# Performance work log

Hardware: AMD Instinct MI355X
Metric: run time of the kernel (lower is better)

The kernel has to match this reference:

```python
import jax, jax.numpy as jnp
import numpy as np

N_NODES = 100000
N_EDGES = 3200000
N_GRAPHS = 256
IN_CH = 8
HID = 64


def _gcn_conv(x, W, b, src, dst, n):
    # PyG GCNConv default: add self-loops, symmetric normalization.
    # out_i = sum_{j->i} d_i^-1/2 d_j^-1/2 (xW)_j + (1/d_i)(xW)_i + b
    xw = x @ W                                     # [N, out]
    deg = jax.ops.segment_sum(jnp.ones_like(dst, dtype=xw.dtype), dst,
                              num_segments=n) + 1.0  # +1 for self-loop
    dinv = jax.lax.rsqrt(deg)
    norm = dinv[src] * dinv[dst]                   # [E]
    agg = jax.ops.segment_sum(xw[src] * norm[:, None], dst, num_segments=n)
    agg = agg + xw * (1.0 / deg)[:, None]          # self-loop term (norm = 1/deg)
    return agg + b


def setup_inputs() -> dict:
    key = jax.random.key(0)
    ks = jax.random.split(key, 12)
    x = jax.random.normal(ks[0], (N_NODES, IN_CH), dtype=jnp.float32)
    edge_index = jax.random.randint(ks[1], (2, N_EDGES), 0, N_NODES, dtype=jnp.int64)
    batch = jnp.sort(jax.random.randint(ks[2], (N_NODES,), 0, N_GRAPHS, dtype=jnp.int64))

    def glorot(k, fan_in, fan_out):
        s = jnp.sqrt(2.0 / (fan_in + fan_out)).astype(jnp.float32)
        return jax.random.normal(k, (fan_in, fan_out), dtype=jnp.float32) * s

    return {
        "x": x, "edge_index": edge_index, "batch": batch,
        "W1": glorot(ks[3], IN_CH, HID), "b1": jnp.zeros((HID,), jnp.float32),
        "W2": glorot(ks[4], HID, 2 * HID), "b2": jnp.zeros((2 * HID,), jnp.float32),
        "W3": glorot(ks[5], 2 * HID, HID), "b3": jnp.zeros((HID,), jnp.float32),
        "Wl1": glorot(ks[6], HID, HID // 2), "bl1": jnp.zeros((HID // 2,), jnp.float32),
        "Wl2": glorot(ks[7], HID // 2, 1), "bl2": jnp.zeros((1,), jnp.float32),
    }


def reference(x, edge_index, batch, W1, b1, W2, b2, W3, b3, Wl1, bl1, Wl2, bl2):
    src, dst = edge_index[0], edge_index[1]
    h = jax.nn.relu(_gcn_conv(x, W1, b1, src, dst, N_NODES))
    h = jax.nn.relu(_gcn_conv(h, W2, b2, src, dst, N_NODES))
    h = jax.nn.relu(_gcn_conv(h, W3, b3, src, dst, N_NODES))
    # global mean pool over graphs
    sums = jax.ops.segment_sum(h, batch, num_segments=N_GRAPHS)
    cnts = jax.ops.segment_sum(jnp.ones((N_NODES,), h.dtype), batch, num_segments=N_GRAPHS)
    g = sums / jnp.maximum(cnts, 1.0)[:, None]     # [G, HID]
    g = jax.nn.relu(g @ Wl1 + bl1)
    out = g @ Wl2 + bl2                            # [G, 1]
    return out[:, 0]
```

## Files before the change

### kernel.cpp

```cpp
#include <hip/hip_runtime.h>
#include <hip/hip_bf16.h>

#define N_NODES 100000
#define N_EDGES 3200000
#define N_GRAPHS 256
#define NB_BUCKETS 196
#define BSHIFT 9
#define NBLK 256
#define SCAN_BLKS 49
#define CSR_CAP 22528

#define OFF_SUMS      0u
#define OFF_CNTF      65536u
#define ZERO_BYTES    66560u
#define OFF_HIST      66560u
#define OFF_BSUM      267264u
#define OFF_ROWPTR    267776u
#define OFF_DINV      668160u
#define OFF_COL       1068544u
#define OFF_XS1       13868544u
#define OFF_BUFQ      20268544u
#define OFF_BUFR      45868544u
#define OFF_BUFP      71468544u
#define OFF_PAIRS     OFF_BUFP

__device__ __forceinline__ unsigned short f2bf(float f) {
    unsigned u = __float_as_uint(f);
    return (unsigned short)((u + 0x7fffu + ((u >> 16) & 1u)) >> 16);
}

__device__ __forceinline__ void acc_bf8(uint4 v, float m, float* a) {
    a[0] += m * __uint_as_float(v.x << 16);
    a[1] += m * __uint_as_float(v.x & 0xffff0000u);
    a[2] += m * __uint_as_float(v.y << 16);
    a[3] += m * __uint_as_float(v.y & 0xffff0000u);
    a[4] += m * __uint_as_float(v.z << 16);
    a[5] += m * __uint_as_float(v.z & 0xffff0000u);
    a[6] += m * __uint_as_float(v.w << 16);
    a[7] += m * __uint_as_float(v.w & 0xffff0000u);
}

__global__ __launch_bounds__(256) void hist_kernel(const int* __restrict__ dst,
                                                   int* __restrict__ hist,
                                                   int* __restrict__ zbase,
                                                   int E, int epb) {
    __shared__ int h[NB_BUCKETS];
    int t = threadIdx.x, blk = blockIdx.x;
    int gid = blk * 256 + t;
    if (gid < (int)(ZERO_BYTES / 4)) zbase[gid] = 0;
    if (t < NB_BUCKETS) h[t] = 0;
    __syncthreads();
    int e0 = blk * epb, e1 = min(e0 + epb, E);
    for (int e = e0 + t; e < e1; e += 256)
        atomicAdd(&h[__builtin_nontemporal_load(&dst[e]) >> BSHIFT], 1);
    __syncthreads();
    if (t < NB_BUCKETS) hist[t * NBLK + blk] = h[t];
}

__global__ __launch_bounds__(1024) void scanhA_kernel(int* __restrict__ hist,
                                                      int* __restrict__ bsum) {
    __shared__ int s[1024];
    int t = threadIdx.x;
    int i = blockIdx.x * 1024 + t;
    int v = hist[i];
    s[t] = v;
    __syncthreads();
    for (int off = 1; off < 1024; off <<= 1) {
        int add = (t >= off) ? s[t - off] : 0;
        __syncthreads();
        s[t] += add;
        __syncthreads();
    }
    hist[i] = s[t] - v;
    if (t == 1023) bsum[blockIdx.x] = s[t];
}

__global__ __launch_bounds__(256) void bin_kernel(const int* __restrict__ src,
                                                  const int* __restrict__ dst,
                                                  const int* __restrict__ hist,
                                                  const int* __restrict__ bsum,
                                                  int* __restrict__ packed, int E, int epb) {
    __shared__ int cur[NB_BUCKETS];
    __shared__ int boffL[SCAN_BLKS];
    int t = threadIdx.x, blk = blockIdx.x;
    if (t < 64) {
        int orig = (t < SCAN_BLKS) ? bsum[t] : 0;
        int v = orig;
        for (int off = 1; off < 64; off <<= 1) {
            int up = __shfl_up(v, off);
            if (t >= off) v += up;
        }
        if (t < SCAN_BLKS) boffL[t] = v - orig;
    }
    __syncthreads();
    if (t < NB_BUCKETS) {
        int i = t * NBLK + blk;
        cur[t] = hist[i] + boffL[i >> 10];
    }
    __syncthreads();
    int e0 = blk * epb, e1 = min(e0 + epb, E);
    for (int e = e0 + t; e < e1; e += 256) {
        int d = __builtin_nontemporal_load(&dst[e]);
        int sv = __builtin_nontemporal_load(&src[e]);
        int pos = atomicAdd(&cur[d >> BSHIFT], 1);
        packed[pos] = ((d & 511) << 17) | sv;
    }
}

__global__ __launch_bounds__(512) void csr_kernel(const int* __restrict__ packed,
                                                  const int* __restrict__ hist,
                                                  const int* __restrict__ bsum,
                                                  const float* __restrict__ x,
                                                  int* __restrict__ row_ptr,
                                                  float* __restrict__ dinv,
                                                  unsigned short* __restrict__ xs1,
                                                  int* __restrict__ col, int E) {
    __shared__ int cntL[512];
    __shared__ int rsL[512];
    __shared__ int fillL[512];
    __shared__ int boffL[SCAN_BLKS];
    __shared__ int srcL[CSR_CAP];
    int t = threadIdx.x, b = blockIdx.x;
    int lo = b << BSHIFT;
    int nloc = min(512, N_NODES - lo);
    cntL[t] = 0;
    fillL[t] = 0;
    if (t < 64) {
        int orig = (t < SCAN_BLKS) ? bsum[t] : 0;
        int v = orig;
        for (int off = 1; off < 64; off <<= 1) {
            int up = __shfl_up(v, off);
            if (t >= off) v += up;
        }
        if (t < SCAN_BLKS) boffL[t] = v - orig;
    }
    __syncthreads();
    int i0 = b * NBLK;
    int start = hist[i0] + boffL[i0 >> 10];
    int end;
    if (b == NB_BUCKETS - 1) end = E;
    else {
        int i1 = (b + 1) * NBLK;
        end = hist[i1] + boffL[i1 >> 10];
    }
    for (int e = start + t; e < end; e += 512)
        atomicAdd(&cntL[packed[e] >> 17], 1);
    __syncthreads();
    int v = cntL[t];
    __syncthreads();
    for (int off = 1; off < 512; off <<= 1) {
        int add = (t >= off) ? cntL[t - off] : 0;
        __syncthreads();
        cntL[t] += add;
        __syncthreads();
    }
    int rowstart = start + cntL[t] - v;
    rsL[t] = rowstart;
    if (t < nloc) {
        int node = lo + t;
        row_ptr[node] = rowstart;
        float d = rsqrtf((float)(v + 1));
        dinv[node] = d;
        const float4* xv = reinterpret_cast<const float4*>(x) + node * 2;
        float4 xa = xv[0], xb = xv[1];
        uint4 p;
        p.x = (unsigned)f2bf(xa.x * d) | ((unsigned)f2bf(xa.y * d) << 16);
        p.y = (unsigned)f2bf(xa.z * d) | ((unsigned)f2bf(xa.w * d) << 16);
        p.z = (unsigned)f2bf(xb.x * d) | ((unsigned)f2bf(xb.y * d) << 16);
        p.w = (unsigned)f2bf(xb.z * d) | ((unsigned)f2bf(xb.w * d) << 16);
        *reinterpret_cast<uint4*>(&xs1[node * 8]) = p;
    }
    if (b == NB_BUCKETS - 1 && t == 0) row_ptr[N_NODES] = E;
    __syncthreads();
    for (int e = start + t; e < end; e += 512) {
        int p = packed[e];
        int dl = p >> 17;
        int pos = rsL[dl] + atomicAdd(&fillL[dl], 1);
        int rel = pos - start;
        if (rel < CSR_CAP) srcL[rel] = p & 0x1FFFF;
        else col[pos] = p & 0x1FFFF;
    }
    __syncthreads();
    int lim = min(end - start, CSR_CAP);
    for (int i = t; i < lim; i += 512)
        col[start + i] = srcL[i];
}

__global__ __launch_bounds__(256) void agg8g1_kernel(
        const unsigned short* __restrict__ xs, const int* __restrict__ row_ptr,
        const int* __restrict__ col, const float* __restrict__ dinv,
        const float* __restrict__ W1, const float* __restrict__ b1,
        unsigned short* __restrict__ xs2, int n) {
    int wave = threadIdx.x >> 6;
    int node = blockIdx.x * 4 + wave;
    if (node >= n) return;
    int lane = threadIdx.x & 63;
    float w[8];
    float bias = b1[lane];
#pragma unroll
    for (int k = 0; k < 8; ++k) w[k] = W1[k * 64 + lane];
    int e0 = row_ptr[node], e1 = row_ptr[node + 1];
    float a[8] = {0.f, 0.f, 0.f, 0.f, 0.f, 0.f, 0.f, 0.f};
    uint4 sv = *reinterpret_cast<const uint4*>(&xs[node * 8]);
    int base = e0;
    for (; base + 64 <= e1; base += 64) {
        int c = __builtin_nontemporal_load(&col[base + lane]);
        uint4 v = *reinterpret_cast<const uint4*>(&xs[c * 8]);
        acc_bf8(v, 1.f, a);
    }
    if (base < e1) {
        int e = base + lane;
        int c = __builtin_nontemporal_load(&col[min(e, e1 - 1)]);
        uint4 v = *reinterpret_cast<const uint4*>(&xs[c * 8]);
        acc_bf8(v, (e < e1) ? 1.f : 0.f, a);
    }
    acc_bf8(sv, (lane == 0) ? 1.f : 0.f, a);
#pragma unroll
    for (int k = 0; k < 8; ++k) {
        a[k] += __shfl_xor(a[k], 1);
        a[k] += __shfl_xor(a[k], 2);
        a[k] += __shfl_xor(a[k], 4);
    }
    float v8 = a[lane & 7];
    v8 += __shfl_xor(v8, 8);
    v8 += __shfl_xor(v8, 16);
    v8 += __shfl_xor(v8, 32);
    float d = dinv[node];
    float acc = bias;
#pragma unroll
    for (int k = 0; k < 8; ++k) acc += (__shfl(v8, k) * d) * w[k];
    xs2[node * 64 + lane] = f2bf(d * fmaxf(acc, 0.0f));
}

template <bool BF16OUT>
__global__ __launch_bounds__(256) void agg64bf_kernel(
        const unsigned short* __restrict__ xs, const int* __restrict__ row_ptr,
        const int* __restrict__ col, const float* __restrict__ dinv,
        float* __restrict__ z, int n) {
    int wave = threadIdx.x >> 6;
    int node = blockIdx.x * 4 + wave;
    if (node >= n) return;
    int lane = threadIdx.x & 63;
    int j = lane >> 3, l = lane & 7;
    int e0 = row_ptr[node], e1 = row_ptr[node + 1];
    float a[8] = {0.f, 0.f, 0.f, 0.f, 0.f, 0.f, 0.f, 0.f};
    uint4 sv = *reinterpret_cast<const uint4*>(&xs[node * 64 + 8 * l]);
    int base = e0;
    for (; e1 - base > 48; base += 32) {
        int s0 = __builtin_nontemporal_load(&col[base + j]);
        int s1 = __builtin_nontemporal_load(&col[base + 8 + j]);
        int s2 = __builtin_nontemporal_load(&col[base + 16 + j]);
        int s3 = __builtin_nontemporal_load(&col[base + 24 + j]);
        uint4 v0 = *reinterpret_cast<const uint4*>(&xs[s0 * 64 + 8 * l]);
        uint4 v1 = *reinterpret_cast<const uint4*>(&xs[s1 * 64 + 8 * l]);
        uint4 v2 = *reinterpret_cast<const uint4*>(&xs[s2 * 64 + 8 * l]);
        uint4 v3 = *reinterpret_cast<const uint4*>(&xs[s3 * 64 + 8 * l]);
        acc_bf8(v0, 1.f, a); acc_bf8(v1, 1.f, a);
        acc_bf8(v2, 1.f, a); acc_bf8(v3, 1.f, a);
    }
    int rem = e1 - base;
    if (rem > 0) {
        int e1m1 = e1 - 1;
        bool g4 = rem > 32, g5 = rem > 40;
        int i0 = base + j,      i1 = base + 8 + j;
        int i2 = base + 16 + j, i3 = base + 24 + j;
        int i4 = base + 32 + j, i5 = base + 40 + j;
        int c0 = __builtin_nontemporal_load(&col[min(i0, e1m1)]);
        int c1 = __builtin_nontemporal_load(&col[min(i1, e1m1)]);
        int c2 = __builtin_nontemporal_load(&col[min(i2, e1m1)]);
        int c3 = __builtin_nontemporal_load(&col[min(i3, e1m1)]);
        int c4 = 0, c5 = 0;
        if (g4) c4 = __builtin_nontemporal_load(&col[min(i4, e1m1)]);
        if (g5) c5 = __builtin_nontemporal_load(&col[min(i5, e1m1)]);
        uint4 v0 = *reinterpret_cast<const uint4*>(&xs[c0 * 64 + 8 * l]);
        uint4 v1 = *reinterpret_cast<const uint4*>(&xs[c1 * 64 + 8 * l]);
        uint4 v2 = *reinterpret_cast<const uint4*>(&xs[c2 * 64 + 8 * l]);
        uint4 v3 = *reinterpret_cast<const uint4*>(&xs[c3 * 64 + 8 * l]);
        uint4 v4, v5;
        if (g4) v4 = *reinterpret_cast<const uint4*>(&xs[c4 * 64 + 8 * l]);
        if (g5) v5 = *reinterpret_cast<const uint4*>(&xs[c5 * 64 + 8 * l]);
        acc_bf8(v0, (i0 < e1) ? 1.f : 0.f, a);
        acc_bf8(v1, (i1 < e1) ? 1.f : 0.f, a);
        acc_bf8(v2, (i2 < e1) ? 1.f : 0.f, a);
        acc_bf8(v3, (i3 < e1) ? 1.f : 0.f, a);
        if (g4) acc_bf8(v4, (i4 < e1) ? 1.f : 0.f, a);
        if (g5) acc_bf8(v5, (i5 < e1) ? 1.f : 0.f, a);
    }
    acc_bf8(sv, (j == 0) ? 1.f : 0.f, a);
#pragma unroll
    for (int k = 0; k < 8; ++k) {
        a[k] += __shfl_xor(a[k], 8);
        a[k] += __shfl_xor(a[k], 16);
        a[k] += __shfl_xor(a[k], 32);
    }
    if (j == 0) {
        float d = dinv[node];
        if constexpr (BF16OUT) {
            unsigned short* zh = reinterpret_cast<unsigned short*>(z);
            uint4 p;
            p.x = (unsigned)f2bf(a[0] * d) | ((unsigned)f2bf(a[1] * d) << 16);
            p.y = (unsigned)f2bf(a[2] * d) | ((unsigned)f2bf(a[3] * d) << 16);
            p.z = (unsigned)f2bf(a[4] * d) | ((unsigned)f2bf(a[5] * d) << 16);
            p.w = (unsigned)f2bf(a[6] * d) | ((unsigned)f2bf(a[7] * d) << 16);
            *reinterpret_cast<uint4*>(&zh[node * 64 + 8 * l]) = p;
        } else {
            float4 r0 = {a[0] * d, a[1] * d, a[2] * d, a[3] * d};
            float4 r1 = {a[4] * d, a[5] * d, a[6] * d, a[7] * d};
            *reinterpret_cast<float4*>(&z[node * 64 + 8 * l]) = r0;
            *reinterpret_cast<float4*>(&z[node * 64 + 8 * l + 4]) = r1;
        }
    }
}

template <int K, int M, bool BIAS, bool RELU, bool SCALE, bool BF16IN, bool BF16OUT>
__global__ __launch_bounds__(256) void gemm_kernel(
        const float* __restrict__ X, const float* __restrict__ W,
        const float* __restrict__ b, const float* __restrict__ dinv,
        float* __restrict__ Y, int nrows) {
    constexpr int CG = M / 4;
    constexpr int RG = 256 / CG;
    constexpr int ROWS = RG * 4;
    constexpr int XSTR = K + 4;
    __shared__ float Wl[K * M];
    __shared__ float Xl[ROWS * XSTR];
    __shared__ float Bl[M];
    int tid = threadIdx.x;
    {
        const float4* Wv = reinterpret_cast<const float4*>(W);
        float4* Wlv = reinterpret_cast<float4*>(Wl);
        for (int i = tid; i < K * M / 4; i += 256) Wlv[i] = Wv[i];
    }
    if (tid < M) Bl[tid] = BIAS ? b[tid] : 0.0f;
    int cg = tid % CG;
    int rg = tid / CG;
    int ntiles = (nrows + ROWS - 1) / ROWS;
    for (int tile = blockIdx.x; tile < ntiles; tile += gridDim.x) {
        int row0 = tile * ROWS;
        __syncthreads();
        {
            int base4 = row0 * (K / 4);
            int tot4 = nrows * (K / 4);
            for (int i = tid; i < ROWS * K / 4; i += 256) {
                float4 v = {0.f, 0.f, 0.f, 0.f};
                if (base4 + i < tot4) {
                    if constexpr (BF16IN) {
                        uint2 raw = reinterpret_cast<const uint2*>(X)[base4 + i];
                        v.x = __uint_as_float(raw.x << 16);
                        v.y = __uint_as_float(raw.x & 0xffff0000u);
                        v.z = __uint_as_float(raw.y << 16);
                        v.w = __uint_as_float(raw.y & 0xffff0000u);
                    } else {
                        v = reinterpret_cast<const float4*>(X)[base4 + i];
                    }
                }
                int rr = i / (K / 4), kk = i % (K / 4);
                *reinterpret_cast<float4*>(&Xl[rr * XSTR + kk * 4]) = v;
            }
        }
        __syncthreads();
        float4 acc[4];
#pragma unroll
        for (int rr = 0; rr < 4; ++rr)
            acc[rr] = *reinterpret_cast<const float4*>(&Bl[cg * 4]);
#pragma unroll 1
        for (int k = 0; k < K; k += 4) {
            const float4 w0 = *reinterpret_cast<const float4*>(&Wl[(k + 0) * M + cg * 4]);
            const float4 w1 = *reinterpret_cast<const float4*>(&Wl[(k + 1) * M + cg * 4]);
            const float4 w2 = *reinterpret_cast<const float4*>(&Wl[(k + 2) * M + cg * 4]);
            const float4 w3 = *reinterpret_cast<const float4*>(&Wl[(k + 3) * M + cg * 4]);
#pragma unroll
            for (int rr = 0; rr < 4; ++rr) {
                const float4 xv = *reinterpret_cast<const float4*>(
                    &Xl[(rg * 4 + rr) * XSTR + k]);
                acc[rr].x += xv.x * w0.x + xv.y * w1.x + xv.z * w2.x + xv.w * w3.x;
                acc[rr].y += xv.x * w0.y + xv.y * w1.y + xv.z * w2.y + xv.w * w3.y;
                acc[rr].z += xv.x * w0.z + xv.y * w1.z + xv.z * w2.z + xv.w * w3.z;
                acc[rr].w += xv.x * w0.w + xv.y * w1.w + xv.z * w2.w + xv.w * w3.w;
            }
        }
#pragma unroll
        for (int rr = 0; rr < 4; ++rr) {
            int row = row0 + rg * 4 + rr;
            if (row < nrows) {
                float4 a = acc[rr];
                if constexpr (RELU) {
                    a.x = fmaxf(a.x, 0.f); a.y = fmaxf(a.y, 0.f);
                    a.z = fmaxf(a.z, 0.f); a.w = fmaxf(a.w, 0.f);
                }
                if constexpr (SCALE) {
                    float d = dinv[row];
                    a.x *= d; a.y *= d; a.z *= d; a.w *= d;
                }
                if constexpr (BF16OUT) {
                    unsigned short* Yh = reinterpret_cast<unsigned short*>(Y);
                    uint2 p;
                    p.x = (unsigned)f2bf(a.x) | ((unsigned)f2bf(a.y) << 16);
                    p.y = (unsigned)f2bf(a.z) | ((unsigned)f2bf(a.w) << 16);
                    *reinterpret_cast<uint2*>(&Yh[row * M + cg * 4]) = p;
                } else {
                    *reinterpret_cast<float4*>(&Y[row * M + cg * 4]) = a;
                }
            }
        }
    }
}

#define POOL_NPB 128
__global__ __launch_bounds__(256) void pool_kernel(
        const float* __restrict__ z3, const float* __restrict__ b3,
        const int* __restrict__ batch, float* __restrict__ sums,
        float* __restrict__ cntf, int n) {
    int wave = threadIdx.x >> 6;
    int lane = threadIdx.x & 63;
    int node0 = blockIdx.x * POOL_NPB + wave * 32;
    int nodeEnd = min(node0 + 32, n);
    if (node0 >= n) return;
    float bias = b3[lane];
    float acc = 0.0f, cnt = 0.0f;
    int curg = -1;
    for (int node = node0; node < nodeEnd; ++node) {
        int g = batch[node];
        if (g != curg) {
            if (curg >= 0) {
                atomicAdd(&sums[curg * 64 + lane], acc);
                if (lane == 0) atomicAdd(&cntf[curg], cnt);
            }
            curg = g; acc = 0.0f; cnt = 0.0f;
        }
        acc += fmaxf(__builtin_nontemporal_load(&z3[node * 64 + lane]) + bias, 0.0f);
        cnt += 1.0f;
    }
    if (curg >= 0) {
        atomicAdd(&sums[curg * 64 + lane], acc);
        if (lane == 0) atomicAdd(&cntf[curg], cnt);
    }
}

__global__ void mlp_kernel(const float* __restrict__ sums, const float* __restrict__ cntf,
                           const float* __restrict__ Wl1, const float* __restrict__ bl1,
                           const float* __restrict__ Wl2, const float* __restrict__ bl2,
                           float* __restrict__ out) {
    __shared__ float gv[64];
    __shared__ float hid[32];
    int g = blockIdx.x, t = threadIdx.x;
    float denom = fmaxf(cntf[g], 1.0f);
    gv[t] = sums[g * 64 + t] / denom;
    __syncthreads();
    if (t < 32) {
        float a = bl1[t];
#pragma unroll
        for (int k = 0; k < 64; ++k) a += gv[k] * Wl1[k * 32 + t];
        hid[t] = fmaxf(a, 0.0f);
    }
    __syncthreads();
    if (t == 0) {
        float o = bl2[0];
#pragma unroll
        for (int k = 0; k < 32; ++k) o += hid[k] * Wl2[k];
        out[g] = o;
    }
}

extern "C" void kernel_launch(void* const* d_in, const int* in_sizes, int n_in,
                              void* d_out, int out_size, void* d_ws, size_t ws_size,
                              hipStream_t stream) {
    const float* x   = (const float*)d_in[0];
    const int* ei    = (const int*)d_in[1];
    const int* batch = (const int*)d_in[2];
    const float* W1  = (const float*)d_in[3];
    const float* b1  = (const float*)d_in[4];
    const float* W2  = (const float*)d_in[5];
    const float* b2  = (const float*)d_in[6];
    const float* W3  = (const float*)d_in[7];
    const float* b3  = (const float*)d_in[8];
    const float* Wl1 = (const float*)d_in[9];
    const float* bl1 = (const float*)d_in[10];
    const float* Wl2 = (const float*)d_in[11];
    const float* bl2 = (const float*)d_in[12];
    float* out = (float*)d_out;

    const int N = N_NODES;
    const int E = in_sizes[1] / 2;
    const int* src = ei;
    const int* dst = ei + E;

    char* ws = (char*)d_ws;
    float* sums    = (float*)(ws + OFF_SUMS);
    float* cntf    = (float*)(ws + OFF_CNTF);
    int*   hist    = (int*)(ws + OFF_HIST);
    int*   bsum    = (int*)(ws + OFF_BSUM);
    int*   row_ptr = (int*)(ws + OFF_ROWPTR);
    float* dinv    = (float*)(ws + OFF_DINV);
    int*   col     = (int*)(ws + OFF_COL);
    unsigned short* xs1 = (unsigned short*)(ws + OFF_XS1);
    float* bufQ    = (float*)(ws + OFF_BUFQ);
    float* bufR    = (float*)(ws + OFF_BUFR);
    float* bufP    = (float*)(ws + OFF_BUFP);
    int*   packed  = (int*)(ws + OFF_PAIRS);

    int epb = (E + NBLK - 1) / NBLK;
    hist_kernel<<<NBLK, 256, 0, stream>>>(dst, hist, (int*)ws, E, epb);
    scanhA_kernel<<<SCAN_BLKS, 1024, 0, stream>>>(hist, bsum);
    bin_kernel<<<NBLK, 256, 0, stream>>>(src, dst, hist, bsum, packed, E, epb);
    csr_kernel<<<NB_BUCKETS, 512, 0, stream>>>(packed, hist, bsum, x,
                                               row_ptr, dinv, xs1, col, E);

    agg8g1_kernel<<<(N + 3) / 4, 256, 0, stream>>>(xs1, row_ptr, col, dinv, W1, b1,
                                                   (unsigned short*)bufQ, N);

    agg64bf_kernel<true><<<(N + 3) / 4, 256, 0, stream>>>(
        (const unsigned short*)bufQ, row_ptr, col, dinv, bufR, N);
    gemm_kernel<64, 128, true, true, false, true, true><<<3125, 256, 0, stream>>>(
        bufR, W2, b2, nullptr, bufP, N);

    gemm_kernel<128, 64, false, false, true, true, true><<<1563, 256, 0, stream>>>(
        bufP, W3, nullptr, dinv, bufR, N);
    agg64bf_kernel<false><<<(N + 3) / 4, 256, 0, stream>>>(
        (const unsigned short*)bufR, row_ptr, col, dinv, bufQ, N);

    pool_kernel<<<(N + POOL_NPB - 1) / POOL_NPB, 256, 0, stream>>>(bufQ, b3, batch, sums, cntf, N);
    mlp_kernel<<<N_GRAPHS, 64, 0, stream>>>(sums, cntf, Wl1, bl1, Wl2, bl2, out);
}
```

Baseline: 405.9 us.

## Replace two-level bucketed CSR build with global-atomic degree count and scatter

Replaces the bucket histogram, bin and per-bucket LDS CSR construction with a direct scheme. Per-node degrees are counted with global atomics, a two-level prefix scan produces row pointers, and a scatter kernel places each edge's source through a per-node atomic cursor. This removes the intermediate packed buffer and the LDS sort pass, but it adds millions of scattered global atomics and random column writes. It also adds more kernel launches and makes the order of columns within each row nondeterministic.

```diff
diff --git a/kernel.cpp b/kernel.cpp
--- a/kernel.cpp
+++ b/kernel.cpp
@@ -4,25 +4,21 @@
 #define N_NODES 100000
 #define N_EDGES 3200000
 #define N_GRAPHS 256
-#define NB_BUCKETS 196
-#define BSHIFT 9
-#define NBLK 256
-#define SCAN_BLKS 49
-#define CSR_CAP 22528
+#define SCAN1_BLKS 98
 
 #define OFF_SUMS      0u
 #define OFF_CNTF      65536u
-#define ZERO_BYTES    66560u
-#define OFF_HIST      66560u
-#define OFF_BSUM      267264u
-#define OFF_ROWPTR    267776u
-#define OFF_DINV      668160u
-#define OFF_COL       1068544u
-#define OFF_XS1       13868544u
+#define OFF_DEG       66560u
+#define ZERO_BYTES    466576u
+#define OFF_BSUM2     466576u
+#define OFF_ROWPTR    467088u
+#define OFF_CURS      867104u
+#define OFF_DINV      1267104u
+#define OFF_COL       1667104u
+#define OFF_XS1       14467104u
 #define OFF_BUFQ      20268544u
 #define OFF_BUFR      45868544u
 #define OFF_BUFP      71468544u
-#define OFF_PAIRS     OFF_BUFP
 
 __device__ __forceinline__ unsigned short f2bf(float f) {
     unsigned u = __float_as_uint(f);
@@ -40,29 +36,25 @@
     a[7] += m * __uint_as_float(v.w & 0xffff0000u);
 }
 
-__global__ __launch_bounds__(256) void hist_kernel(const int* __restrict__ dst,
-                                                   int* __restrict__ hist,
-                                                   int* __restrict__ zbase,
-                                                   int E, int epb) {
-    __shared__ int h[NB_BUCKETS];
-    int t = threadIdx.x, blk = blockIdx.x;
-    int gid = blk * 256 + t;
+__global__ __launch_bounds__(256) void zero_kernel(int* __restrict__ zbase) {
+    int gid = blockIdx.x * 256 + threadIdx.x;
     if (gid < (int)(ZERO_BYTES / 4)) zbase[gid] = 0;
-    if (t < NB_BUCKETS) h[t] = 0;
-    __syncthreads();
-    int e0 = blk * epb, e1 = min(e0 + epb, E);
-    for (int e = e0 + t; e < e1; e += 256)
-        atomicAdd(&h[__builtin_nontemporal_load(&dst[e]) >> BSHIFT], 1);
-    __syncthreads();
-    if (t < NB_BUCKETS) hist[t * NBLK + blk] = h[t];
-}
-
-__global__ __launch_bounds__(1024) void scanhA_kernel(int* __restrict__ hist,
-                                                      int* __restrict__ bsum) {
+}
+
+__global__ __launch_bounds__(256) void deg_kernel(const int* __restrict__ dst,
+                                                  int* __restrict__ deg, int E) {
+    int stride = gridDim.x * 256;
+    for (int e = blockIdx.x * 256 + threadIdx.x; e < E; e += stride)
+        atomicAdd(&deg[__builtin_nontemporal_load(&dst[e])], 1);
+}
+
+__global__ __launch_bounds__(1024) void scan1_kernel(const int* __restrict__ deg,
+                                                     int* __restrict__ rp,
+                                                     int* __restrict__ bsum, int n) {
     __shared__ int s[1024];
     int t = threadIdx.x;
     int i = blockIdx.x * 1024 + t;
-    int v = hist[i];
+    int v = (i < n) ? deg[i] : 0;
     s[t] = v;
     __syncthreads();
     for (int off = 1; off < 1024; off <<= 1) {
@@ -71,119 +63,64 @@
         s[t] += add;
         __syncthreads();
     }
-    hist[i] = s[t] - v;
+    if (i < n) rp[i] = s[t] - v;
     if (t == 1023) bsum[blockIdx.x] = s[t];
 }
 
-__global__ __launch_bounds__(256) void bin_kernel(const int* __restrict__ src,
-                                                  const int* __restrict__ dst,
-                                                  const int* __restrict__ hist,
-                                                  const int* __restrict__ bsum,
-                                                  int* __restrict__ packed, int E, int epb) {
-    __shared__ int cur[NB_BUCKETS];
-    __shared__ int boffL[SCAN_BLKS];
+__global__ __launch_bounds__(128) void scan2_kernel(int* __restrict__ bsum) {
+    __shared__ int s[128];
+    int t = threadIdx.x;
+    int v = (t < SCAN1_BLKS) ? bsum[t] : 0;
+    s[t] = v;
+    __syncthreads();
+    for (int off = 1; off < 128; off <<= 1) {
+        int add = (t >= off) ? s[t - off] : 0;
+        __syncthreads();
+        s[t] += add;
+        __syncthreads();
+    }
+    if (t < SCAN1_BLKS) bsum[t] = s[t] - v;
+}
+
+__global__ __launch_bounds__(1024) void fin_kernel(const int* __restrict__ bsum,
+                                                   const int* __restrict__ deg,
+                                                   const float* __restrict__ x,
+                                                   int* __restrict__ rp,
+                                                   int* __restrict__ cursor,
+                                                   float* __restrict__ dinv,
+                                                   unsigned short* __restrict__ xs1,
+                                                   int n, int E) {
     int t = threadIdx.x, blk = blockIdx.x;
-    if (t < 64) {
-        int orig = (t < SCAN_BLKS) ? bsum[t] : 0;
-        int v = orig;
-        for (int off = 1; off < 64; off <<= 1) {
-            int up = __shfl_up(v, off);
-            if (t >= off) v += up;
-        }
-        if (t < SCAN_BLKS) boffL[t] = v - orig;
-    }
-    __syncthreads();
-    if (t < NB_BUCKETS) {
-        int i = t * NBLK + blk;
-        cur[t] = hist[i] + boffL[i >> 10];
-    }
-    __syncthreads();
-    int e0 = blk * epb, e1 = min(e0 + epb, E);
-    for (int e = e0 + t; e < e1; e += 256) {
-        int d = __builtin_nontemporal_load(&dst[e]);
-        int sv = __builtin_nontemporal_load(&src[e]);
-        int pos = atomicAdd(&cur[d >> BSHIFT], 1);
-        packed[pos] = ((d & 511) << 17) | sv;
-    }
-}
-
-__global__ __launch_bounds__(512) void csr_kernel(const int* __restrict__ packed,
-                                                  const int* __restrict__ hist,
-                                                  const int* __restrict__ bsum,
-                                                  const float* __restrict__ x,
-                                                  int* __restrict__ row_ptr,
-                                                  float* __restrict__ dinv,
-                                                  unsigned short* __restrict__ xs1,
-                                                  int* __restrict__ col, int E) {
-    __shared__ int cntL[512];
-    __shared__ int rsL[512];
-    __shared__ int fillL[512];
-    __shared__ int boffL[SCAN_BLKS];
-    __shared__ int srcL[CSR_CAP];
-    int t = threadIdx.x, b = blockIdx.x;
-    int lo = b << BSHIFT;
-    int nloc = min(512, N_NODES - lo);
-    cntL[t] = 0;
-    fillL[t] = 0;
-    if (t < 64) {
-        int orig = (t < SCAN_BLKS) ? bsum[t] : 0;
-        int v = orig;
-        for (int off = 1; off < 64; off <<= 1) {
-            int up = __shfl_up(v, off);
-            if (t >= off) v += up;
-        }
-        if (t < SCAN_BLKS) boffL[t] = v - orig;
-    }
-    __syncthreads();
-    int i0 = b * NBLK;
-    int start = hist[i0] + boffL[i0 >> 10];
-    int end;
-    if (b == NB_BUCKETS - 1) end = E;
-    else {
-        int i1 = (b + 1) * NBLK;
-        end = hist[i1] + boffL[i1 >> 10];
-    }
-    for (int e = start + t; e < end; e += 512)
-        atomicAdd(&cntL[packed[e] >> 17], 1);
-    __syncthreads();
-    int v = cntL[t];
-    __syncthreads();
-    for (int off = 1; off < 512; off <<= 1) {
-        int add = (t >= off) ? cntL[t - off] : 0;
-        __syncthreads();
-        cntL[t] += add;
-        __syncthreads();
-    }
-    int rowstart = start + cntL[t] - v;
-    rsL[t] = rowstart;
-    if (t < nloc) {
-        int node = lo + t;
-        row_ptr[node] = rowstart;
-        float d = rsqrtf((float)(v + 1));
-        dinv[node] = d;
-        const float4* xv = reinterpret_cast<const float4*>(x) + node * 2;
+    int i = blk * 1024 + t;
+    if (i < n) {
+        int rpv = rp[i] + bsum[blk];
+        rp[i] = rpv;
+        cursor[i] = rpv;
+        float d = rsqrtf((float)(deg[i] + 1));
+        dinv[i] = d;
+        const float4* xv = reinterpret_cast<const float4*>(x) + i * 2;
         float4 xa = xv[0], xb = xv[1];
         uint4 p;
         p.x = (unsigned)f2bf(xa.x * d) | ((unsigned)f2bf(xa.y * d) << 16);
         p.y = (unsigned)f2bf(xa.z * d) | ((unsigned)f2bf(xa.w * d) << 16);
         p.z = (unsigned)f2bf(xb.x * d) | ((unsigned)f2bf(xb.y * d) << 16);
         p.w = (unsigned)f2bf(xb.z * d) | ((unsigned)f2bf(xb.w * d) << 16);
-        *reinterpret_cast<uint4*>(&xs1[node * 8]) = p;
-    }
-    if (b == NB_BUCKETS - 1 && t == 0) row_ptr[N_NODES] = E;
-    __syncthreads();
-    for (int e = start + t; e < end; e += 512) {
-        int p = packed[e];
-        int dl = p >> 17;
-        int pos = rsL[dl] + atomicAdd(&fillL[dl], 1);
-        int rel = pos - start;
-        if (rel < CSR_CAP) srcL[rel] = p & 0x1FFFF;
-        else col[pos] = p & 0x1FFFF;
-    }
-    __syncthreads();
-    int lim = min(end - start, CSR_CAP);
-    for (int i = t; i < lim; i += 512)
-        col[start + i] = srcL[i];
+        *reinterpret_cast<uint4*>(&xs1[i * 8]) = p;
+    }
+    if (i == 0) rp[n] = E;
+}
+
+__global__ __launch_bounds__(256) void scatter_kernel(const int* __restrict__ src,
+                                                      const int* __restrict__ dst,
+                                                      int* __restrict__ cursor,
+                                                      int* __restrict__ col, int E) {
+    int stride = gridDim.x * 256;
+    for (int e = blockIdx.x * 256 + threadIdx.x; e < E; e += stride) {
+        int d = __builtin_nontemporal_load(&dst[e]);
+        int s = __builtin_nontemporal_load(&src[e]);
+        int pos = atomicAdd(&cursor[d], 1);
+        __builtin_nontemporal_store(s, &col[pos]);
+    }
 }
 
 __global__ __launch_bounds__(256) void agg8g1_kernel(
@@ -487,23 +424,24 @@
     char* ws = (char*)d_ws;
     float* sums    = (float*)(ws + OFF_SUMS);
     float* cntf    = (float*)(ws + OFF_CNTF);
-    int*   hist    = (int*)(ws + OFF_HIST);
-    int*   bsum    = (int*)(ws + OFF_BSUM);
+    int*   deg     = (int*)(ws + OFF_DEG);
+    int*   bsum2   = (int*)(ws + OFF_BSUM2);
     int*   row_ptr = (int*)(ws + OFF_ROWPTR);
+    int*   cursor  = (int*)(ws + OFF_CURS);
     float* dinv    = (float*)(ws + OFF_DINV);
     int*   col     = (int*)(ws + OFF_COL);
     unsigned short* xs1 = (unsigned short*)(ws + OFF_XS1);
     float* bufQ    = (float*)(ws + OFF_BUFQ);
     float* bufR    = (float*)(ws + OFF_BUFR);
     float* bufP    = (float*)(ws + OFF_BUFP);
-    int*   packed  = (int*)(ws + OFF_PAIRS);
-
-    int epb = (E + NBLK - 1) / NBLK;
-    hist_kernel<<<NBLK, 256, 0, stream>>>(dst, hist, (int*)ws, E, epb);
-    scanhA_kernel<<<SCAN_BLKS, 1024, 0, stream>>>(hist, bsum);
-    bin_kernel<<<NBLK, 256, 0, stream>>>(src, dst, hist, bsum, packed, E, epb);
-    csr_kernel<<<NB_BUCKETS, 512, 0, stream>>>(packed, hist, bsum, x,
-                                               row_ptr, dinv, xs1, col, E);
+
+    zero_kernel<<<456, 256, 0, stream>>>((int*)ws);
+    deg_kernel<<<1024, 256, 0, stream>>>(dst, deg, E);
+    scan1_kernel<<<SCAN1_BLKS, 1024, 0, stream>>>(deg, row_ptr, bsum2, N);
+    scan2_kernel<<<1, 128, 0, stream>>>(bsum2);
+    fin_kernel<<<SCAN1_BLKS, 1024, 0, stream>>>(bsum2, deg, x, row_ptr, cursor,
+                                                dinv, xs1, N, E);
+    scatter_kernel<<<1024, 256, 0, stream>>>(src, dst, cursor, col, E);
 
     agg8g1_kernel<<<(N + 3) / 4, 256, 0, stream>>>(xs1, row_ptr, col, dinv, W1, b1,
                                                    (unsigned short*)bufQ, N);
```

Measured after the change: 728.3 us. 79.4% more time.

## Replace FP32 SIMT GEMMs with bf16 MFMA matrix-core GEMMs

Applied to the files above, without the earlier changes.

Replaces the shared-memory FP32 FMA GEMM for the layer-2 and layer-3 dense transforms with a kernel using the bf16 16x16x32 MFMA instruction. Each wave loads A fragments directly from global memory, and the weights are converted to bf16 and transposed into LDS per block. The goal is to cut the ALU cost of the two dense GEMMs. Weights are now also rounded to bf16, which adds precision loss. The aggregation kernel gains an unused node-range parameter.

```diff
diff --git a/kernel.cpp b/kernel.cpp
--- a/kernel.cpp
+++ b/kernel.cpp
@@ -23,6 +23,9 @@
 #define OFF_BUFR      45868544u
 #define OFF_BUFP      71468544u
 #define OFF_PAIRS     OFF_BUFP
+
+typedef __attribute__((ext_vector_type(8))) short bf16x8;
+typedef __attribute__((ext_vector_type(4))) float f32x4;
 
 __device__ __forceinline__ unsigned short f2bf(float f) {
     unsigned u = __float_as_uint(f);
@@ -236,10 +239,10 @@
 __global__ __launch_bounds__(256) void agg64bf_kernel(
         const unsigned short* __restrict__ xs, const int* __restrict__ row_ptr,
         const int* __restrict__ col, const float* __restrict__ dinv,
-        float* __restrict__ z, int n) {
+        float* __restrict__ z, int n0, int n1) {
     int wave = threadIdx.x >> 6;
-    int node = blockIdx.x * 4 + wave;
-    if (node >= n) return;
+    int node = n0 + blockIdx.x * 4 + wave;
+    if (node >= n1) return;
     int lane = threadIdx.x & 63;
     int j = lane >> 3, l = lane & 7;
     int e0 = row_ptr[node], e1 = row_ptr[node + 1];
@@ -312,94 +315,59 @@
     }
 }
 
-template <int K, int M, bool BIAS, bool RELU, bool SCALE, bool BF16IN, bool BF16OUT>
-__global__ __launch_bounds__(256) void gemm_kernel(
-        const float* __restrict__ X, const float* __restrict__ W,
+template <int K, int M, bool BIAS, bool RELU, bool SCALE, bool BF16OUT>
+__global__ __launch_bounds__(256) void mgemm_kernel(
+        const unsigned short* __restrict__ X, const float* __restrict__ W,
         const float* __restrict__ b, const float* __restrict__ dinv,
         float* __restrict__ Y, int nrows) {
-    constexpr int CG = M / 4;
-    constexpr int RG = 256 / CG;
-    constexpr int ROWS = RG * 4;
-    constexpr int XSTR = K + 4;
-    __shared__ float Wl[K * M];
-    __shared__ float Xl[ROWS * XSTR];
-    __shared__ float Bl[M];
+    constexpr int KP = K + 8;
+    constexpr int NT = M / 16;
+    constexpr int KS = K / 32;
+    __shared__ unsigned short Wt[M * KP];
     int tid = threadIdx.x;
-    {
-        const float4* Wv = reinterpret_cast<const float4*>(W);
-        float4* Wlv = reinterpret_cast<float4*>(Wl);
-        for (int i = tid; i < K * M / 4; i += 256) Wlv[i] = Wv[i];
-    }
-    if (tid < M) Bl[tid] = BIAS ? b[tid] : 0.0f;
-    int cg = tid % CG;
-    int rg = tid / CG;
-    int ntiles = (nrows + ROWS - 1) / ROWS;
-    for (int tile = blockIdx.x; tile < ntiles; tile += gridDim.x) {
-        int row0 = tile * ROWS;
-        __syncthreads();
-        {
-            int base4 = row0 * (K / 4);
-            int tot4 = nrows * (K / 4);
-            for (int i = tid; i < ROWS * K / 4; i += 256) {
-                float4 v = {0.f, 0.f, 0.f, 0.f};
-                if (base4 + i < tot4) {
-                    if constexpr (BF16IN) {
-                        uint2 raw = reinterpret_cast<const uint2*>(X)[base4 + i];
-                        v.x = __uint_as_float(raw.x << 16);
-                        v.y = __uint_as_float(raw.x & 0xffff0000u);
-                        v.z = __uint_as_float(raw.y << 16);
-                        v.w = __uint_as_float(raw.y & 0xffff0000u);
-                    } else {
-                        v = reinterpret_cast<const float4*>(X)[base4 + i];
-                    }
-                }
-                int rr = i / (K / 4), kk = i % (K / 4);
-                *reinterpret_cast<float4*>(&Xl[rr * XSTR + kk * 4]) = v;
-            }
-        }
-        __syncthreads();
-        float4 acc[4];
-#pragma unroll
-        for (int rr = 0; rr < 4; ++rr)
-            acc[rr] = *reinterpret_cast<const float4*>(&Bl[cg * 4]);
-#pragma unroll 1
-        for (int k = 0; k < K; k += 4) {
-            const float4 w0 = *reinterpret_cast<const float4*>(&Wl[(k + 0) * M + cg * 4]);
-            const float4 w1 = *reinterpret_cast<const float4*>(&Wl[(k + 1) * M + cg * 4]);
-            const float4 w2 = *reinterpret_cast<const float4*>(&Wl[(k + 2) * M + cg * 4]);
-            const float4 w3 = *reinterpret_cast<const float4*>(&Wl[(k + 3) * M + cg * 4]);
-#pragma unroll
-            for (int rr = 0; rr < 4; ++rr) {
-                const float4 xv = *reinterpret_cast<const float4*>(
-                    &Xl[(rg * 4 + rr) * XSTR + k]);
-                acc[rr].x += xv.x * w0.x + xv.y * w1.x + xv.z * w2.x + xv.w * w3.x;
-                acc[rr].y += xv.x * w0.y + xv.y * w1.y + xv.z * w2.y + xv.w * w3.y;
-                acc[rr].z += xv.x * w0.z + xv.y * w1.z + xv.z * w2.z + xv.w * w3.z;
-                acc[rr].w += xv.x * w0.w + xv.y * w1.w + xv.z * w2.w + xv.w * w3.w;
-            }
-        }
-#pragma unroll
-        for (int rr = 0; rr < 4; ++rr) {
-            int row = row0 + rg * 4 + rr;
-            if (row < nrows) {
-                float4 a = acc[rr];
-                if constexpr (RELU) {
-                    a.x = fmaxf(a.x, 0.f); a.y = fmaxf(a.y, 0.f);
-                    a.z = fmaxf(a.z, 0.f); a.w = fmaxf(a.w, 0.f);
-                }
-                if constexpr (SCALE) {
-                    float d = dinv[row];
-                    a.x *= d; a.y *= d; a.z *= d; a.w *= d;
-                }
-                if constexpr (BF16OUT) {
-                    unsigned short* Yh = reinterpret_cast<unsigned short*>(Y);
-                    uint2 p;
-                    p.x = (unsigned)f2bf(a.x) | ((unsigned)f2bf(a.y) << 16);
-                    p.y = (unsigned)f2bf(a.z) | ((unsigned)f2bf(a.w) << 16);
-                    *reinterpret_cast<uint2*>(&Yh[row * M + cg * 4]) = p;
-                } else {
-                    *reinterpret_cast<float4*>(&Y[row * M + cg * 4]) = a;
-                }
+    for (int i = tid; i < K * M; i += 256) {
+        int k = i / M, m = i % M;
+        Wt[m * KP + k] = f2bf(W[i]);
+    }
+    __syncthreads();
+    int wave = tid >> 6, lane = tid & 63;
+    int row0 = blockIdx.x * 64 + wave * 16;
+    int hl = lane >> 4, ll = lane & 15;
+    int arow = min(row0 + ll, nrows - 1);
+    bf16x8 afrag[KS];
+#pragma unroll
+    for (int ks = 0; ks < KS; ++ks)
+        afrag[ks] = *reinterpret_cast<const bf16x8*>(&X[arow * K + ks * 32 + hl * 8]);
+    f32x4 acc[NT];
+#pragma unroll
+    for (int nt = 0; nt < NT; ++nt) {
+        float bv = BIAS ? b[nt * 16 + ll] : 0.0f;
+        acc[nt] = {bv, bv, bv, bv};
+    }
+#pragma unroll
+    for (int nt = 0; nt < NT; ++nt) {
+#pragma unroll
+        for (int ks = 0; ks < KS; ++ks) {
+            bf16x8 bfrag = *reinterpret_cast<const bf16x8*>(
+                &Wt[(nt * 16 + ll) * KP + ks * 32 + hl * 8]);
+            acc[nt] = __builtin_amdgcn_mfma_f32_16x16x32_bf16(
+                afrag[ks], bfrag, acc[nt], 0, 0, 0);
+        }
+    }
+#pragma unroll
+    for (int r = 0; r < 4; ++r) {
+        int row = row0 + hl * 4 + r;
+        if (row < nrows) {
+            float d = SCALE ? dinv[row] : 1.0f;
+#pragma unroll
+            for (int nt = 0; nt < NT; ++nt) {
+                float v = acc[nt][r];
+                if constexpr (RELU) v = fmaxf(v, 0.0f);
+                if constexpr (SCALE) v *= d;
+                if constexpr (BF16OUT)
+                    reinterpret_cast<unsigned short*>(Y)[row * M + nt * 16 + ll] = f2bf(v);
+                else
+                    Y[row * M + nt * 16 + ll] = v;
             }
         }
     }
@@ -509,14 +477,14 @@
                                                    (unsigned short*)bufQ, N);
 
     agg64bf_kernel<true><<<(N + 3) / 4, 256, 0, stream>>>(
-        (const unsigned short*)bufQ, row_ptr, col, dinv, bufR, N);
-    gemm_kernel<64, 128, true, true, false, true, true><<<3125, 256, 0, stream>>>(
-        bufR, W2, b2, nullptr, bufP, N);
-
-    gemm_kernel<128, 64, false, false, true, true, true><<<1563, 256, 0, stream>>>(
-        bufP, W3, nullptr, dinv, bufR, N);
+        (const unsigned short*)bufQ, row_ptr, col, dinv, bufR, 0, N);
+    mgemm_kernel<64, 128, true, true, false, true><<<1563, 256, 0, stream>>>(
+        (const unsigned short*)bufR, W2, b2, nullptr, bufP, N);
+
+    mgemm_kernel<128, 64, false, false, true, true><<<1563, 256, 0, stream>>>(
+        (const unsigned short*)bufP, W3, nullptr, dinv, bufR, N);
     agg64bf_kernel<false><<<(N + 3) / 4, 256, 0, stream>>>(
-        (const unsigned short*)bufR, row_ptr, col, dinv, bufQ, N);
+        (const unsigned short*)bufR, row_ptr, col, dinv, bufQ, 0, N);
 
     pool_kernel<<<(N + POOL_NPB - 1) / POOL_NPB, 256, 0, stream>>>(bufQ, b3, batch, sums, cntf, N);
     mlp_kernel<<<N_GRAPHS, 64, 0, stream>>>(sums, cntf, Wl1, bl1, Wl2, bl2, out);
```

New measurement: 356.2 us. 12.3% less time.
